# Kernel tuning notes

Measured on AMD Instinct MI355X. Metric: run time of the kernel, lower is better.

The kernel has to match this reference:

```python
import jax, jax.numpy as jnp
import numpy as np

B, L, D, H, W = 32, 1024, 512, 8, 5  # batch, seq, d_model, heads, local_context_length
DK = D // H


def _local_mix(x, W0, b0, w):
    """Sliding-window local-context weighting (faithful to the torch loop version).
    Pads front with w-1 zeros, applies linear (so padded rows become the bias),
    softmax-weights each length-w causal window against the current position,
    and sums the window.  x: [B, L, D] -> [B, L, D]."""
    Bb, Ll, Dd = x.shape
    xp = jnp.pad(x, ((0, 0), (w - 1, 0), (0, 0)))          # [B, L+w-1, D]
    xp = xp @ W0 + b0                                       # linear AFTER pad (padded rows = bias)
    idx = jnp.arange(Ll)[:, None] + jnp.arange(w)[None, :]  # [L, w] window indices into padded seq
    win = xp[:, idx, :]                                     # [B, L, w, D]
    cur = xp[:, w - 1:, :]                                  # [B, L, D] current positions
    scores = jnp.einsum('bld,blwd->blw', cur, win) / jnp.sqrt(jnp.float32(Dd))
    wts = jax.nn.softmax(scores, axis=-1)                   # [B, L, w]
    return jnp.einsum('blw,blwd->bld', wts, win)            # [B, L, D]


def setup_inputs() -> dict:
    rng = jax.random.key(0)
    ks = jax.random.split(rng, 7)
    s = 0.02
    return {
        'query': jax.random.normal(ks[0], (B, L, D), jnp.float32),
        'key':   jax.random.normal(ks[1], (B, L, D), jnp.float32),
        'value': jax.random.normal(ks[2], (B, L, D), jnp.float32),
        'W0':    jax.random.normal(ks[3], (D, D), jnp.float32) * s,
        'b0':    jax.random.normal(ks[4], (D,), jnp.float32) * s,
        'Wout':  jax.random.normal(ks[5], (D, D), jnp.float32) * s,
        'bout':  jax.random.normal(ks[6], (D,), jnp.float32) * s,
    }


def reference(query, key, value, W0, b0, Wout, bout):
    q = _local_mix(query, W0, b0, W).reshape(B, L, H, DK).transpose(0, 2, 1, 3)  # [B,H,L,dk]
    k = _local_mix(key, W0, b0, W).reshape(B, L, H, DK).transpose(0, 2, 1, 3)
    v = (value @ W0 + b0).reshape(B, L, H, DK).transpose(0, 2, 1, 3)
    scores = jnp.einsum('bhqd,bhkd->bhqk', q, k) / jnp.sqrt(jnp.float32(DK))     # [B,H,L,L]
    p = jax.nn.softmax(scores, axis=-1)
    x = jnp.einsum('bhqk,bhkd->bhqd', p, v)
    x = x.transpose(0, 2, 1, 3).reshape(B, L, D)
    return x @ Wout + bout
```

## Files before the change

kernel.cpp:

```cpp
#include <hip/hip_runtime.h>


typedef __attribute__((ext_vector_type(8))) short bf16x8;
typedef __attribute__((ext_vector_type(4))) float f32x4;

#define MFMA16(a, b, c) __builtin_amdgcn_mfma_f32_16x16x32_bf16((a), (b), (c), 0, 0, 0)

static __device__ __forceinline__ float bf2f(unsigned short u) {
  union { unsigned int i; float f; } v; v.i = ((unsigned int)u) << 16; return v.f;
}
static __device__ __forceinline__ unsigned short f2b(float f) {
  union { float fv; unsigned int i; } v; v.fv = f;
  unsigned int u = v.i;
  return (unsigned short)((u + 0x7fffu + ((u >> 16) & 1u)) >> 16);
}
static __device__ __forceinline__ unsigned int cvtpk(float lo, float hi) {
  unsigned int r;
  asm("v_cvt_pk_bf16_f32 %0, %1, %2" : "=v"(r) : "v"(lo), "v"(hi));
  return r;
}
static __device__ __forceinline__ void barrier_lgkm() {
  asm volatile("s_waitcnt lgkmcnt(0)" ::: "memory");
  __builtin_amdgcn_s_barrier();
  __builtin_amdgcn_sched_barrier(0);
}

__global__ __launch_bounds__(256) void tcast2_k(const float* __restrict__ s0,
                                                unsigned short* __restrict__ d0,
                                                const float* __restrict__ s1,
                                                unsigned short* __restrict__ d1) {
  int i = blockIdx.x * 256 + threadIdx.x;
  const float* s = s0;
  unsigned short* d = d0;
  if (i >= 262144) { i -= 262144; s = s1; d = d1; }
  int k = i >> 9, n = i & 511;
  d[(size_t)n * 512 + k] = f2b(s[(size_t)k * 512 + n]);
}

template <int AMODE, int OUTMODE>
__device__ __forceinline__ void gemm_body(const void* __restrict__ A_,
                                          const unsigned short* __restrict__ BT,
                                          const float* __restrict__ bias,
                                          void* __restrict__ out_, int bm, int bn) {
  __shared__ unsigned short As[2][128 * 32];
  __shared__ unsigned short Bs[2][128 * 32];
  const int tid = threadIdx.x;
  const int w = tid >> 6, l = tid & 63;
  const int lg = l >> 4, lr = l & 15;
  const int wr = w >> 1, wc = w & 1;
  const int rowbase = bm * 128;
  const int colbase0 = bn * 128;
  const int colbase = colbase0 + wc * 64;

  const int srow = w * 32 + (l >> 1);
  const int ks = l & 1;
  const int sswz = (l >> 2) & 3;
  const int p0 = (2 * ks) ^ sswz, p1 = (2 * ks + 1) ^ sswz;

  f32x4 acc[4][4];
#pragma unroll
  for (int m = 0; m < 4; ++m)
#pragma unroll
    for (int n = 0; n < 4; ++n) acc[m][n] = (f32x4){0.f, 0.f, 0.f, 0.f};

  float4 fa0[4], fa1[4];
  uint4 ba0[2], ba1[2];
  uint4 bb[2];

  auto loadAf = [&](int kt, float4* d) {
    const float* p = (const float*)A_ + (size_t)(rowbase + srow) * 512 + kt * 32 + ks * 16;
    d[0] = ((const float4*)p)[0]; d[1] = ((const float4*)p)[1];
    d[2] = ((const float4*)p)[2]; d[3] = ((const float4*)p)[3];
  };
  auto loadAb = [&](int kt, uint4* d) {
    const unsigned short* p = (const unsigned short*)A_ + (size_t)(rowbase + srow) * 512 + kt * 32 + ks * 16;
    d[0] = ((const uint4*)p)[0]; d[1] = ((const uint4*)p)[1];
  };
  auto loadB = [&](int kt) {
    const unsigned short* p = BT + (size_t)(colbase0 + srow) * 512 + kt * 32 + ks * 16;
    bb[0] = ((const uint4*)p)[0]; bb[1] = ((const uint4*)p)[1];
  };
  auto writeAf = [&](int buf, const float4* d) {
    uint4 u0, u1;
    u0.x = cvtpk(d[0].x, d[0].y); u0.y = cvtpk(d[0].z, d[0].w);
    u0.z = cvtpk(d[1].x, d[1].y); u0.w = cvtpk(d[1].z, d[1].w);
    u1.x = cvtpk(d[2].x, d[2].y); u1.y = cvtpk(d[2].z, d[2].w);
    u1.z = cvtpk(d[3].x, d[3].y); u1.w = cvtpk(d[3].z, d[3].w);
    *(uint4*)&As[buf][srow * 32 + p0 * 8] = u0;
    *(uint4*)&As[buf][srow * 32 + p1 * 8] = u1;
  };
  auto writeAb = [&](int buf, const uint4* d) {
    *(uint4*)&As[buf][srow * 32 + p0 * 8] = d[0];
    *(uint4*)&As[buf][srow * 32 + p1 * 8] = d[1];
  };
  auto writeB = [&](int buf) {
    *(uint4*)&Bs[buf][srow * 32 + p0 * 8] = bb[0];
    *(uint4*)&Bs[buf][srow * 32 + p1 * 8] = bb[1];
  };

  if constexpr (AMODE == 0) { loadAf(0, fa0); } else { loadAb(0, ba0); }
  loadB(0);
  if constexpr (AMODE == 0) writeAf(0, fa0); else writeAb(0, ba0);
  writeB(0);
  if constexpr (AMODE == 0) { loadAf(1, fa1); } else { loadAb(1, ba1); }
  barrier_lgkm();

  const int rsw = ((lr >> 1) & 3);

#pragma unroll
  for (int kt = 0; kt < 16; ++kt) {
    const int cur = kt & 1;
    bf16x8 af[4], bf[4];
#pragma unroll
    for (int m = 0; m < 4; ++m) {
      const int r = wr * 64 + m * 16 + lr;
      af[m] = *(const bf16x8*)&As[cur][r * 32 + ((lg ^ rsw) << 3)];
    }
#pragma unroll
    for (int n = 0; n < 4; ++n) {
      const int c = wc * 64 + n * 16 + lr;
      bf[n] = *(const bf16x8*)&Bs[cur][c * 32 + ((lg ^ rsw) << 3)];
    }
    if (kt < 15) loadB(kt + 1);
    if (kt < 14) {
      if constexpr (AMODE == 0) { if (cur == 0) loadAf(kt + 2, fa0); else loadAf(kt + 2, fa1); }
      else                      { if (cur == 0) loadAb(kt + 2, ba0); else loadAb(kt + 2, ba1); }
    }
    __builtin_amdgcn_s_setprio(1);
#pragma unroll
    for (int m = 0; m < 4; ++m)
#pragma unroll
      for (int n = 0; n < 4; ++n) acc[m][n] = MFMA16(af[m], bf[n], acc[m][n]);
    __builtin_amdgcn_s_setprio(0);
    if (kt < 15) {
      if constexpr (AMODE == 0) { if (cur == 0) writeAf(1, fa1); else writeAf(0, fa0); }
      else                      { if (cur == 0) writeAb(1, ba1); else writeAb(0, ba0); }
      writeB(cur ^ 1);
      barrier_lgkm();
    }
  }

#pragma unroll
  for (int m = 0; m < 4; ++m)
#pragma unroll
    for (int n = 0; n < 4; ++n) {
      const int grow0 = rowbase + wr * 64 + m * 16 + 4 * lg;
      const int gcol = colbase + n * 16 + lr;
      const float bs = bias[gcol];
#pragma unroll
      for (int r = 0; r < 4; ++r) {
        float v = acc[m][n][r] + bs;
        if constexpr (OUTMODE == 0)
          ((unsigned short*)out_)[(size_t)(grow0 + r) * 512 + gcol] = f2b(v);
        else
          ((float*)out_)[(size_t)(grow0 + r) * 512 + gcol] = v;
      }
    }
}

__global__ __launch_bounds__(256) void proj3_k(const float* __restrict__ q,
                                               const float* __restrict__ k,
                                               const float* __restrict__ v,
                                               const unsigned short* __restrict__ W0T,
                                               const float* __restrict__ b0,
                                               unsigned short* __restrict__ Pq,
                                               unsigned short* __restrict__ Pk,
                                               unsigned short* __restrict__ Pv) {
  const int wg = (blockIdx.x & 7) * 384 + (blockIdx.x >> 3);
  const int t = wg >> 10, rem = wg & 1023;
  const float* A = t == 0 ? q : t == 1 ? k : v;
  unsigned short* O = t == 0 ? Pq : t == 1 ? Pk : Pv;
  gemm_body<0, 0>(A, W0T, b0, O, rem >> 2, rem & 3);
}

__global__ __launch_bounds__(256) void gemmout_k(const unsigned short* __restrict__ A,
                                                 const unsigned short* __restrict__ WoT,
                                                 const float* __restrict__ bout,
                                                 float* __restrict__ out) {
  const int wg = (blockIdx.x & 7) * 128 + (blockIdx.x >> 3);
  gemm_body<1, 1>(A, WoT, bout, out, wg >> 2, wg & 3);
}

__global__ __launch_bounds__(256) void localmix2_k(const unsigned short* __restrict__ Pq,
                                                   const unsigned short* __restrict__ Pk,
                                                   const float* __restrict__ b0,
                                                   unsigned short* __restrict__ Qm,
                                                   unsigned short* __restrict__ Km) {
  const int w = threadIdx.x >> 6, lane = threadIdx.x & 63;
  const int pp = blockIdx.x * 4 + w;
  const unsigned short* P;
  unsigned short* out;
  float outscale;
  int p;
  if (pp < 32768) { P = Pq; out = Qm; outscale = 0.18033688011112042f; p = pp; }
  else            { P = Pk; out = Km; outscale = 1.0f; p = pp - 32768; }
  const int l = p & 1023;
  const int d0 = lane * 8;

  float win[5][8];
#pragma unroll
  for (int j = 0; j < 5; ++j) {
    const int src = l - 4 + j;
    if (src >= 0) {
      const uint4 v = *(const uint4*)(P + (size_t)(p - 4 + j) * 512 + d0);
      const unsigned short* u = (const unsigned short*)&v;
#pragma unroll
      for (int i = 0; i < 8; ++i) win[j][i] = bf2f(u[i]);
    } else {
      const float4 f0 = *(const float4*)(b0 + d0);
      const float4 f1 = *(const float4*)(b0 + d0 + 4);
      win[j][0] = f0.x; win[j][1] = f0.y; win[j][2] = f0.z; win[j][3] = f0.w;
      win[j][4] = f1.x; win[j][5] = f1.y; win[j][6] = f1.z; win[j][7] = f1.w;
    }
  }
  float s[5];
#pragma unroll
  for (int j = 0; j < 5; ++j) {
    float t = 0.f;
#pragma unroll
    for (int i = 0; i < 8; ++i) t += win[4][i] * win[j][i];
    s[j] = t;
  }
#pragma unroll
  for (int off = 1; off < 64; off <<= 1)
#pragma unroll
    for (int j = 0; j < 5; ++j) s[j] += __shfl_xor(s[j], off, 64);
  const float sc = 0.04419417382415922f;
  float mx = -1e30f;
#pragma unroll
  for (int j = 0; j < 5; ++j) { s[j] *= sc; mx = fmaxf(mx, s[j]); }
  float e[5], sum = 0.f;
#pragma unroll
  for (int j = 0; j < 5; ++j) { e[j] = __expf(s[j] - mx); sum += e[j]; }
  const float inv = 1.f / sum;
  __attribute__((ext_vector_type(8))) unsigned short o;
#pragma unroll
  for (int i = 0; i < 8; ++i) {
    float a = 0.f;
#pragma unroll
    for (int j = 0; j < 5; ++j) a += e[j] * win[j][i];
    o[i] = f2b(a * inv * outscale);
  }
  *(__attribute__((ext_vector_type(8))) unsigned short*)(out + (size_t)p * 512 + d0) = o;
}

__global__ __launch_bounds__(256) void attn_k(const unsigned short* __restrict__ Q,
                                              const unsigned short* __restrict__ K,
                                              const unsigned short* __restrict__ V,
                                              unsigned short* __restrict__ AO) {
  __shared__ unsigned short Ks[2][64 * 64];
  __shared__ unsigned short Vt[2][64 * 64];
  const int tid = threadIdx.x;
  const int w = tid >> 6, l = tid & 63;
  const int lg = l >> 4, lr = l & 15;
  const int wg = (blockIdx.x & 7) * 256 + (blockIdx.x >> 3);
  const int qt = wg & 7, bh = wg >> 3;
  const int h = bh & 7, b = bh >> 3;
  const size_t base = (size_t)(b * 1024) * 512 + h * 64;
  const unsigned short* Qb = Q + base + (size_t)(qt * 128) * 512;
  const unsigned short* Kb = K + base;
  const unsigned short* Vb = V + base;

  bf16x8 qf[2][2];
#pragma unroll
  for (int rb = 0; rb < 2; ++rb)
#pragma unroll
    for (int ks = 0; ks < 2; ++ks)
      qf[rb][ks] = *(const bf16x8*)(Qb + (size_t)(w * 32 + rb * 16 + lr) * 512 + ks * 32 + lg * 8);

  f32x4 acc[2][4];
#pragma unroll
  for (int rb = 0; rb < 2; ++rb)
#pragma unroll
    for (int nb = 0; nb < 4; ++nb) acc[rb][nb] = (f32x4){0.f, 0.f, 0.f, 0.f};
  float lrun[2] = {0.f, 0.f};

  const int sk_row = tid >> 2, sk_seg = tid & 3;
  const int sv_key = tid & 63, sv_d0 = (tid >> 6) * 16;
  const int vpos = (sv_key & 32) + ((sv_key >> 2) & 3) * 8 + ((sv_key >> 4) & 1) * 4 + (sv_key & 3);
  const int vpg = vpos >> 3, vpw = vpos & 7;
  const int r7 = sk_row & 7;

  uint4 kr0, kr1, vr0, vr1;
  auto loadT = [&](int t) {
    const uint4* ksrc = (const uint4*)(Kb + (size_t)(t * 64 + sk_row) * 512 + sk_seg * 16);
    kr0 = ksrc[0]; kr1 = ksrc[1];
    const uint4* vsrc = (const uint4*)(Vb + (size_t)(t * 64 + sv_key) * 512 + sv_d0);
    vr0 = vsrc[0]; vr1 = vsrc[1];
  };
  auto writeT = [&](int bufi) {
    unsigned short* kd = Ks[bufi];
    unsigned short* vd = Vt[bufi];
    *(uint4*)&kd[sk_row * 64 + (((2 * sk_seg) ^ r7) << 3)] = kr0;
    *(uint4*)&kd[sk_row * 64 + (((2 * sk_seg + 1) ^ r7) << 3)] = kr1;
    const unsigned short* u0 = (const unsigned short*)&vr0;
    const unsigned short* u1 = (const unsigned short*)&vr1;
#pragma unroll
    for (int j = 0; j < 8; ++j) {
      vd[(sv_d0 + j) * 64 + (((vpg ^ j) << 3) | vpw)] = u0[j];
      vd[(sv_d0 + 8 + j) * 64 + (((vpg ^ j) << 3) | vpw)] = u1[j];
    }
  };

  loadT(0);
  writeT(0);
  loadT(1);
  barrier_lgkm();

  const int swz0 = (lg ^ (lr & 7)) << 3, swz1 = ((4 + lg) ^ (lr & 7)) << 3;

  for (int it = 0; it < 16; ++it) {
    const int cur = it & 1;
    f32x4 sf[2][4];
    __builtin_amdgcn_s_setprio(1);
#pragma unroll
    for (int kb = 0; kb < 4; ++kb) {
      const int krow = (kb * 16 + lr) * 64;
      bf16x8 kf0 = *(const bf16x8*)&Ks[cur][krow + swz0];
      bf16x8 kf1 = *(const bf16x8*)&Ks[cur][krow + swz1];
#pragma unroll
      for (int rb = 0; rb < 2; ++rb) {
        f32x4 z = (f32x4){0.f, 0.f, 0.f, 0.f};
        z = MFMA16(kf0, qf[rb][0], z);
        z = MFMA16(kf1, qf[rb][1], z);
        sf[rb][kb] = z;
      }
    }
    __builtin_amdgcn_s_setprio(0);

    if (it < 15) writeT((it + 1) & 1);
    if (it < 14) loadT(it + 2);

#pragma unroll
    for (int rb = 0; rb < 2; ++rb) {
#pragma unroll
      for (int kb = 0; kb < 4; ++kb)
#pragma unroll
        for (int r = 0; r < 4; ++r)
          sf[rb][kb][r] = __builtin_amdgcn_exp2f(sf[rb][kb][r]);
      float s0 = (sf[rb][0][0] + sf[rb][0][1]) + (sf[rb][0][2] + sf[rb][0][3]);
      float s1 = (sf[rb][1][0] + sf[rb][1][1]) + (sf[rb][1][2] + sf[rb][1][3]);
      float s2 = (sf[rb][2][0] + sf[rb][2][1]) + (sf[rb][2][2] + sf[rb][2][3]);
      float s3 = (sf[rb][3][0] + sf[rb][3][1]) + (sf[rb][3][2] + sf[rb][3][3]);
      float t = (s0 + s1) + (s2 + s3);
      t += __shfl_xor(t, 16, 64);
      t += __shfl_xor(t, 32, 64);
      lrun[rb] += t;
    }

    union { uint4 d; bf16x8 v; } pa[2][2];
#pragma unroll
    for (int rb = 0; rb < 2; ++rb)
#pragma unroll
      for (int t2 = 0; t2 < 2; ++t2) {
        pa[rb][t2].d.x = cvtpk(sf[rb][2 * t2][0], sf[rb][2 * t2][1]);
        pa[rb][t2].d.y = cvtpk(sf[rb][2 * t2][2], sf[rb][2 * t2][3]);
        pa[rb][t2].d.z = cvtpk(sf[rb][2 * t2 + 1][0], sf[rb][2 * t2 + 1][1]);
        pa[rb][t2].d.w = cvtpk(sf[rb][2 * t2 + 1][2], sf[rb][2 * t2 + 1][3]);
      }

    __builtin_amdgcn_s_setprio(1);
#pragma unroll
    for (int t2 = 0; t2 < 2; ++t2) {
      bf16x8 vf[4];
#pragma unroll
      for (int nb = 0; nb < 4; ++nb) {
        const int vrow = (nb * 16 + lr) * 64;
        vf[nb] = *(const bf16x8*)&Vt[cur][vrow + (((4 * t2 + lg) ^ (lr & 7)) << 3)];
      }
#pragma unroll
      for (int rb = 0; rb < 2; ++rb)
#pragma unroll
        for (int nb = 0; nb < 4; ++nb) acc[rb][nb] = MFMA16(pa[rb][t2].v, vf[nb], acc[rb][nb]);
    }
    __builtin_amdgcn_s_setprio(0);
    if (it < 15) barrier_lgkm();
  }

#pragma unroll
  for (int rb = 0; rb < 2; ++rb) {
    const float rec = 1.f / lrun[rb];
    float lv[4];
#pragma unroll
    for (int r = 0; r < 4; ++r) lv[r] = __shfl(rec, lg * 4 + r, 64);
#pragma unroll
    for (int nb = 0; nb < 4; ++nb) {
      const int gcol = nb * 16 + lr;
#pragma unroll
      for (int r = 0; r < 4; ++r) {
        const int grow = qt * 128 + w * 32 + rb * 16 + 4 * lg + r;
        AO[base + (size_t)grow * 512 + gcol] = f2b(acc[rb][nb][r] * lv[r]);
      }
    }
  }
}

extern "C" void kernel_launch(void* const* d_in, const int* in_sizes, int n_in,
                              void* d_out, int out_size, void* d_ws, size_t ws_size,
                              hipStream_t stream) {
  const float* query = (const float*)d_in[0];
  const float* key   = (const float*)d_in[1];
  const float* value = (const float*)d_in[2];
  const float* W0    = (const float*)d_in[3];
  const float* b0    = (const float*)d_in[4];
  const float* Wout  = (const float*)d_in[5];
  const float* bout  = (const float*)d_in[6];
  float* out = (float*)d_out;

  char* ws = (char*)d_ws;
  const size_t PSZ = (size_t)32768 * 512 * 2;
  unsigned short* Pq  = (unsigned short*)(ws);
  unsigned short* Pk  = (unsigned short*)(ws + PSZ);
  unsigned short* Pv  = (unsigned short*)(ws + 2 * PSZ);
  unsigned short* Qm  = (unsigned short*)(ws + 3 * PSZ);
  unsigned short* Km  = (unsigned short*)(ws + 4 * PSZ);
  unsigned short* W0T = (unsigned short*)(ws + 5 * PSZ);
  unsigned short* WoT = (unsigned short*)(ws + 5 * PSZ + 524288);

  tcast2_k<<<2048, 256, 0, stream>>>(W0, W0T, Wout, WoT);
  proj3_k<<<3072, 256, 0, stream>>>(query, key, value, W0T, b0, Pq, Pk, Pv);
  localmix2_k<<<16384, 256, 0, stream>>>(Pq, Pk, b0, Qm, Km);
  attn_k<<<2048, 256, 0, stream>>>(Qm, Km, Pv, Pq );
  gemmout_k<<<1024, 256, 0, stream>>>(Pq, WoT, bout, out);
}
```

Before: 317.2 us.

## Make GEMM warps independent with per-warp A tiles and register-loaded B

Restructures the shared GEMM body so each warp owns 32 rows by the full 128-column tile. Each warp stages its own A slice in a private LDS buffer and loads B fragments straight from global memory into registers. This removes the block-wide barriers and the shared B tile, so warps no longer stall waiting on each other. In exchange, B is read from global by every warp (four times per block), per-warp register pressure rises (16 accumulators plus 16 B fragments), and the per-warp LDS writes followed by reads now rely on implicit in-wave ordering rather than an explicit wait.

```diff
diff --git a/kernel.cpp b/kernel.cpp
--- a/kernel.cpp
+++ b/kernel.cpp
@@ -38,34 +38,31 @@
 }
 
 template <int AMODE, int OUTMODE>
-__device__ __forceinline__ void gemm_body(const void* __restrict__ A_,
-                                          const unsigned short* __restrict__ BT,
-                                          const float* __restrict__ bias,
-                                          void* __restrict__ out_, int bm, int bn) {
-  __shared__ unsigned short As[2][128 * 32];
-  __shared__ unsigned short Bs[2][128 * 32];
+__device__ __forceinline__ void gemm_wp(const void* __restrict__ A_,
+                                        const unsigned short* __restrict__ BT,
+                                        const float* __restrict__ bias,
+                                        void* __restrict__ out_, int bm, int bn) {
+  __shared__ unsigned short As[4][2][32 * 32];
   const int tid = threadIdx.x;
   const int w = tid >> 6, l = tid & 63;
   const int lg = l >> 4, lr = l & 15;
-  const int wr = w >> 1, wc = w & 1;
-  const int rowbase = bm * 128;
-  const int colbase0 = bn * 128;
-  const int colbase = colbase0 + wc * 64;
-
-  const int srow = w * 32 + (l >> 1);
-  const int ks = l & 1;
+  const int rowbase = bm * 128 + w * 32;
+  const int colbase = bn * 128;
+
+  const int srow = l >> 1, ks = l & 1;
   const int sswz = (l >> 2) & 3;
-  const int p0 = (2 * ks) ^ sswz, p1 = (2 * ks + 1) ^ sswz;
-
-  f32x4 acc[4][4];
-#pragma unroll
-  for (int m = 0; m < 4; ++m)
-#pragma unroll
-    for (int n = 0; n < 4; ++n) acc[m][n] = (f32x4){0.f, 0.f, 0.f, 0.f};
+  const int g0 = (2 * ks) ^ sswz, g1 = (2 * ks + 1) ^ sswz;
+  const int rswz = (lr >> 1) & 3;
+
+  f32x4 acc[2][8];
+#pragma unroll
+  for (int m = 0; m < 2; ++m)
+#pragma unroll
+    for (int n = 0; n < 8; ++n) acc[m][n] = (f32x4){0.f, 0.f, 0.f, 0.f};
 
   float4 fa0[4], fa1[4];
   uint4 ba0[2], ba1[2];
-  uint4 bb[2];
+  bf16x8 br0[8], br1[8];
 
   auto loadAf = [&](int kt, float4* d) {
     const float* p = (const float*)A_ + (size_t)(rowbase + srow) * 512 + kt * 32 + ks * 16;
@@ -76,9 +73,10 @@
     const unsigned short* p = (const unsigned short*)A_ + (size_t)(rowbase + srow) * 512 + kt * 32 + ks * 16;
     d[0] = ((const uint4*)p)[0]; d[1] = ((const uint4*)p)[1];
   };
-  auto loadB = [&](int kt) {
-    const unsigned short* p = BT + (size_t)(colbase0 + srow) * 512 + kt * 32 + ks * 16;
-    bb[0] = ((const uint4*)p)[0]; bb[1] = ((const uint4*)p)[1];
+  auto loadB = [&](int kt, bf16x8* d) {
+#pragma unroll
+    for (int n = 0; n < 8; ++n)
+      d[n] = *(const bf16x8*)(BT + (size_t)(colbase + n * 16 + lr) * 512 + kt * 32 + lg * 8);
   };
   auto writeAf = [&](int buf, const float4* d) {
     uint4 u0, u1;
@@ -86,65 +84,49 @@
     u0.z = cvtpk(d[1].x, d[1].y); u0.w = cvtpk(d[1].z, d[1].w);
     u1.x = cvtpk(d[2].x, d[2].y); u1.y = cvtpk(d[2].z, d[2].w);
     u1.z = cvtpk(d[3].x, d[3].y); u1.w = cvtpk(d[3].z, d[3].w);
-    *(uint4*)&As[buf][srow * 32 + p0 * 8] = u0;
-    *(uint4*)&As[buf][srow * 32 + p1 * 8] = u1;
+    *(uint4*)&As[w][buf][srow * 32 + g0 * 8] = u0;
+    *(uint4*)&As[w][buf][srow * 32 + g1 * 8] = u1;
   };
   auto writeAb = [&](int buf, const uint4* d) {
-    *(uint4*)&As[buf][srow * 32 + p0 * 8] = d[0];
-    *(uint4*)&As[buf][srow * 32 + p1 * 8] = d[1];
-  };
-  auto writeB = [&](int buf) {
-    *(uint4*)&Bs[buf][srow * 32 + p0 * 8] = bb[0];
-    *(uint4*)&Bs[buf][srow * 32 + p1 * 8] = bb[1];
+    *(uint4*)&As[w][buf][srow * 32 + g0 * 8] = d[0];
+    *(uint4*)&As[w][buf][srow * 32 + g1 * 8] = d[1];
   };
 
   if constexpr (AMODE == 0) { loadAf(0, fa0); } else { loadAb(0, ba0); }
-  loadB(0);
+  loadB(0, br0);
+  if constexpr (AMODE == 0) { loadAf(1, fa1); } else { loadAb(1, ba1); }
   if constexpr (AMODE == 0) writeAf(0, fa0); else writeAb(0, ba0);
-  writeB(0);
-  if constexpr (AMODE == 0) { loadAf(1, fa1); } else { loadAb(1, ba1); }
-  barrier_lgkm();
-
-  const int rsw = ((lr >> 1) & 3);
 
 #pragma unroll
   for (int kt = 0; kt < 16; ++kt) {
     const int cur = kt & 1;
-    bf16x8 af[4], bf[4];
-#pragma unroll
-    for (int m = 0; m < 4; ++m) {
-      const int r = wr * 64 + m * 16 + lr;
-      af[m] = *(const bf16x8*)&As[cur][r * 32 + ((lg ^ rsw) << 3)];
-    }
-#pragma unroll
-    for (int n = 0; n < 4; ++n) {
-      const int c = wc * 64 + n * 16 + lr;
-      bf[n] = *(const bf16x8*)&Bs[cur][c * 32 + ((lg ^ rsw) << 3)];
-    }
-    if (kt < 15) loadB(kt + 1);
     if (kt < 14) {
       if constexpr (AMODE == 0) { if (cur == 0) loadAf(kt + 2, fa0); else loadAf(kt + 2, fa1); }
       else                      { if (cur == 0) loadAb(kt + 2, ba0); else loadAb(kt + 2, ba1); }
     }
-    __builtin_amdgcn_s_setprio(1);
-#pragma unroll
-    for (int m = 0; m < 4; ++m)
-#pragma unroll
-      for (int n = 0; n < 4; ++n) acc[m][n] = MFMA16(af[m], bf[n], acc[m][n]);
-    __builtin_amdgcn_s_setprio(0);
+    if (kt < 15) { if (cur == 0) loadB(kt + 1, br1); else loadB(kt + 1, br0); }
+    bf16x8 af[2];
+#pragma unroll
+    for (int m = 0; m < 2; ++m) {
+      const int r = m * 16 + lr;
+      af[m] = *(const bf16x8*)&As[w][cur][r * 32 + ((lg ^ rswz) << 3)];
+    }
+    const bf16x8* bcur = cur == 0 ? br0 : br1;
+#pragma unroll
+    for (int m = 0; m < 2; ++m)
+#pragma unroll
+      for (int n = 0; n < 8; ++n) acc[m][n] = MFMA16(af[m], bcur[n], acc[m][n]);
     if (kt < 15) {
       if constexpr (AMODE == 0) { if (cur == 0) writeAf(1, fa1); else writeAf(0, fa0); }
       else                      { if (cur == 0) writeAb(1, ba1); else writeAb(0, ba0); }
-      writeB(cur ^ 1);
-      barrier_lgkm();
-    }
-  }
-
-#pragma unroll
-  for (int m = 0; m < 4; ++m)
-#pragma unroll
-    for (int n = 0; n < 4; ++n) {
-      const int grow0 = rowbase + wr * 64 + m * 16 + 4 * lg;
+    }
+  }
+
+#pragma unroll
+  for (int m = 0; m < 2; ++m)
+#pragma unroll
+    for (int n = 0; n < 8; ++n) {
+      const int grow0 = rowbase + m * 16 + 4 * lg;
       const int gcol = colbase + n * 16 + lr;
       const float bs = bias[gcol];
 #pragma unroll
@@ -170,7 +152,7 @@
   const int t = wg >> 10, rem = wg & 1023;
   const float* A = t == 0 ? q : t == 1 ? k : v;
   unsigned short* O = t == 0 ? Pq : t == 1 ? Pk : Pv;
-  gemm_body<0, 0>(A, W0T, b0, O, rem >> 2, rem & 3);
+  gemm_wp<0, 0>(A, W0T, b0, O, rem >> 2, rem & 3);
 }
 
 __global__ __launch_bounds__(256) void gemmout_k(const unsigned short* __restrict__ A,
@@ -178,7 +160,7 @@
                                                  const float* __restrict__ bout,
                                                  float* __restrict__ out) {
   const int wg = (blockIdx.x & 7) * 128 + (blockIdx.x >> 3);
-  gemm_body<1, 1>(A, WoT, bout, out, wg >> 2, wg & 3);
+  gemm_wp<1, 1>(A, WoT, bout, out, wg >> 2, wg & 3);
 }
 
 __global__ __launch_bounds__(256) void localmix2_k(const unsigned short* __restrict__ Pq,
```

Result: slower. 481.6 us (+51.8%).
